# Performance work log

Measured on AMD Instinct MI355X. Metric: run time of the kernel, lower is better.

The kernel has to match this reference:

```python
import jax, jax.numpy as jnp
import numpy as np

DIM = 1024
CTX_DIM = 1024
HEADS = 16
DIM_HEAD = 64
INNER = HEADS * DIM_HEAD  # 1024
FF_INNER = 4 * DIM        # 4096
EPS = 1e-5


def layer_norm(x, g, b):
    mu = jnp.mean(x, axis=-1, keepdims=True)
    var = jnp.var(x, axis=-1, keepdims=True)
    return (x - mu) * jax.lax.rsqrt(var + EPS) * g + b


def setup_inputs() -> dict:
    key = jax.random.key(0)
    ks = jax.random.split(key, 9)
    b, n, j = 4, 2048, 1024
    inp = {
        "x": jax.random.normal(ks[0], (b, n, DIM), dtype=jnp.float32),
        "context": jax.random.normal(ks[1], (b, j, CTX_DIM), dtype=jnp.float32),
        "ln_g": jnp.ones((DIM,), jnp.float32),
        "ln_b": jnp.zeros((DIM,), jnp.float32),
        "cln_g": jnp.ones((CTX_DIM,), jnp.float32),
        "cln_b": jnp.zeros((CTX_DIM,), jnp.float32),
        "Wq": jax.random.normal(ks[2], (DIM, INNER), dtype=jnp.float32) * (DIM ** -0.5),
        "Wkv": jax.random.normal(ks[3], (CTX_DIM, 2 * DIM_HEAD), dtype=jnp.float32) * (CTX_DIM ** -0.5),
        "Wo": jax.random.normal(ks[4], (INNER, DIM), dtype=jnp.float32) * (INNER ** -0.5),
        "Wff1": jax.random.normal(ks[5], (DIM, 2 * FF_INNER), dtype=jnp.float32) * (DIM ** -0.5),
        "Wff2": jax.random.normal(ks[6], (FF_INNER, DIM), dtype=jnp.float32) * (FF_INNER ** -0.5),
    }
    return inp


def reference(x, context, ln_g, ln_b, cln_g, cln_b, Wq, Wkv, Wo, Wff1, Wff2):
    scale = DIM_HEAD ** -0.5
    xn = layer_norm(x, ln_g, ln_b)                       # [b, n, dim]
    cn = layer_norm(context, cln_g, cln_b)               # [b, j, ctx_dim]
    b, n, _ = xn.shape
    q = (xn @ Wq).reshape(b, n, HEADS, DIM_HEAD).transpose(0, 2, 1, 3) * scale  # [b,h,n,d]
    kv = cn @ Wkv                                        # [b, j, 2d]
    k, v = kv[..., :DIM_HEAD], kv[..., DIM_HEAD:]        # [b, j, d] each (shared head)
    sim = jnp.einsum('bhid,bjd->bhij', q, k)
    attn = jax.nn.softmax(sim, axis=-1)
    out = jnp.einsum('bhij,bjd->bhid', attn, v)          # [b,h,n,d]
    out = out.transpose(0, 2, 1, 3).reshape(b, n, INNER) @ Wo  # [b,n,dim]
    # parallel SwiGLU FF on normed x
    ff = xn @ Wff1                                       # [b,n,2*ff_inner]
    h, gate = ff[..., :FF_INNER], ff[..., FF_INNER:]
    out = out + (jax.nn.silu(gate) * h) @ Wff2
    return out
```

## Files before the change

### kernel.cpp

```cpp
#include <hip/hip_runtime.h>
#include <math.h>

typedef unsigned short u16;
typedef __attribute__((ext_vector_type(8))) short short8;
typedef __attribute__((ext_vector_type(8))) unsigned short ushortx8;
typedef __attribute__((ext_vector_type(4))) unsigned short ushortx4;
typedef __attribute__((ext_vector_type(4))) float floatx4;

#define DEVI __device__ __forceinline__

DEVI float bf2f(u16 u) {
    unsigned int i = ((unsigned int)u) << 16;
    float f; __builtin_memcpy(&f, &i, 4); return f;
}
DEVI u16 f2bf(float f) {
    unsigned int i; __builtin_memcpy(&i, &f, 4);
    i += 0x7fffu + ((i >> 16) & 1u);
    return (u16)(i >> 16);
}
DEVI void gl_lds16(const void* g, void* l) {
    __builtin_amdgcn_global_load_lds(
        (const __attribute__((address_space(1))) void*)g,
        (__attribute__((address_space(3))) void*)l, 16, 0, 0);
}

__global__ void transpose_kernel(const float* __restrict__ B, u16* __restrict__ BT,
                                 int K, int N) {
    __shared__ u16 t[32][33];
    int nb = blockIdx.x * 32, kb = blockIdx.y * 32;
    int tx = threadIdx.x, ty = threadIdx.y;
    for (int i = ty; i < 32; i += 8)
        t[i][tx] = f2bf(B[(size_t)(kb + i) * N + nb + tx]);
    __syncthreads();
    for (int i = ty; i < 32; i += 8)
        BT[(size_t)(nb + i) * K + kb + tx] = t[tx][i];
}

__global__ __launch_bounds__(256)
void ln_kernel(const float* __restrict__ x, const float* __restrict__ g,
               const float* __restrict__ b, u16* __restrict__ out) {
    __shared__ float sw[4], sw2[4];
    const int tid = threadIdx.x, wave = tid >> 6, lane = tid & 63;
    const float* xr = x + (size_t)blockIdx.x * 1024;
    float4 v = *(const float4*)(xr + tid * 4);
    float f[4] = {v.x, v.y, v.z, v.w};
    float s = f[0] + f[1] + f[2] + f[3];
    float s2 = f[0]*f[0] + f[1]*f[1] + f[2]*f[2] + f[3]*f[3];
    for (int o = 32; o; o >>= 1) {
        s  += __shfl_xor(s,  o, 64);
        s2 += __shfl_xor(s2, o, 64);
    }
    if (lane == 0) { sw[wave] = s; sw2[wave] = s2; }
    __syncthreads();
    float tot  = sw[0] + sw[1] + sw[2] + sw[3];
    float tot2 = sw2[0] + sw2[1] + sw2[2] + sw2[3];
    float mu  = tot * (1.f / 1024.f);
    float var = tot2 * (1.f / 1024.f) - mu * mu;
    float rs  = rsqrtf(var + 1e-5f);
    float4 gv = *(const float4*)(g + tid * 4);
    float4 bv = *(const float4*)(b + tid * 4);
    ushortx4 ov;
    ov[0] = f2bf((f[0] - mu) * rs * gv.x + bv.x);
    ov[1] = f2bf((f[1] - mu) * rs * gv.y + bv.y);
    ov[2] = f2bf((f[2] - mu) * rs * gv.z + bv.z);
    ov[3] = f2bf((f[3] - mu) * rs * gv.w + bv.w);
    *(ushortx4*)(out + (size_t)blockIdx.x * 1024 + tid * 4) = ov;
}

enum { EPI_PLAIN = 0, EPI_Q = 1, EPI_KV = 2, EPI_ADD_F32 = 3 };

template <int EPI>
__global__ __launch_bounds__(256)
void gemm_bt_kernel(const u16* __restrict__ A, const u16* __restrict__ BT,
                    void* __restrict__ Cv, u16* __restrict__ AUX,
                    int M, int N, int K) {
    __shared__ u16 As[128 * 32];
    __shared__ u16 Bs[128 * 32];
    const int tid = threadIdx.x, wave = tid >> 6, lane = tid & 63;
    const int mbase = blockIdx.x * 128, nbase = blockIdx.y * 128;
    const int m0 = (wave & 1) * 64, n0 = (wave >> 1) * 64;
    const int lrow = lane & 15, lq = lane >> 4;

    floatx4 zero = {0.f, 0.f, 0.f, 0.f};
    floatx4 acc[4][4];
#pragma unroll
    for (int i = 0; i < 4; i++)
#pragma unroll
        for (int j = 0; j < 4; j++) acc[i][j] = zero;

    for (int kt = 0; kt < K; kt += 32) {
#pragma unroll
        for (int i = 0; i < 2; i++) {
            int e = i * 2048 + tid * 8;
            int r = e >> 5, c = e & 31;
            gl_lds16(A  + (size_t)(mbase + r) * K + kt + c, As + e);
            gl_lds16(BT + (size_t)(nbase + r) * K + kt + c, Bs + e);
        }
        __syncthreads();
        short8 af[4], bf[4];
#pragma unroll
        for (int f = 0; f < 4; f++) {
            af[f] = *(const short8*)(As + (m0 + f * 16 + lrow) * 32 + lq * 8);
            bf[f] = *(const short8*)(Bs + (n0 + f * 16 + lrow) * 32 + lq * 8);
        }
#pragma unroll
        for (int i = 0; i < 4; i++)
#pragma unroll
            for (int j = 0; j < 4; j++)
                acc[i][j] = __builtin_amdgcn_mfma_f32_16x16x32_bf16(af[i], bf[j], acc[i][j], 0, 0, 0);
        __syncthreads();
    }

#pragma unroll
    for (int mf = 0; mf < 4; mf++)
#pragma unroll
        for (int nf = 0; nf < 4; nf++)
#pragma unroll
            for (int r = 0; r < 4; r++) {
                int row = mbase + m0 + mf * 16 + lq * 4 + r;
                int col = nbase + n0 + nf * 16 + lrow;
                float v = acc[mf][nf][r];
                if constexpr (EPI == EPI_PLAIN) {
                    ((u16*)Cv)[(size_t)row * N + col] = f2bf(v);
                } else if constexpr (EPI == EPI_Q) {
                    int b = row >> 11, i2 = row & 2047, h = col >> 6, d = col & 63;
                    ((u16*)Cv)[((size_t)((b * 16 + h) * 2048 + i2)) * 64 + d] = f2bf(v * 0.125f);
                } else if constexpr (EPI == EPI_KV) {
                    int b = row >> 10, j = row & 1023;
                    if (col < 64) ((u16*)Cv)[(size_t)row * 64 + col] = f2bf(v);
                    else AUX[((size_t)(b * 64 + (col - 64))) * 1024 + j] = f2bf(v);
                } else {
                    ((float*)Cv)[(size_t)row * N + col] = v + bf2f(AUX[(size_t)row * N + col]);
                }
            }
}

__global__ __launch_bounds__(256)
void gemm_ff1_kernel(const u16* __restrict__ A, const u16* __restrict__ BTh,
                     const u16* __restrict__ BTg, u16* __restrict__ Cact,
                     int K, int Nout) {
    __shared__ u16 As[128 * 32];
    __shared__ u16 Bh[64 * 32];
    __shared__ u16 Bg[64 * 32];
    const int tid = threadIdx.x, wave = tid >> 6, lane = tid & 63;
    const int mbase = blockIdx.x * 128, nbase = blockIdx.y * 64;
    const int m0 = (wave & 1) * 64, n0 = (wave >> 1) * 32;
    const int lrow = lane & 15, lq = lane >> 4;

    floatx4 zero = {0.f, 0.f, 0.f, 0.f};
    floatx4 ah[4][2], ag[4][2];
#pragma unroll
    for (int i = 0; i < 4; i++)
#pragma unroll
        for (int j = 0; j < 2; j++) { ah[i][j] = zero; ag[i][j] = zero; }

    for (int kt = 0; kt < K; kt += 32) {
#pragma unroll
        for (int i = 0; i < 2; i++) {
            int e = i * 2048 + tid * 8;
            int r = e >> 5, c = e & 31;
            gl_lds16(A + (size_t)(mbase + r) * K + kt + c, As + e);
        }
        {
            int e = tid * 8;
            int r = e >> 5, c = e & 31;
            gl_lds16(BTh + (size_t)(nbase + r) * K + kt + c, Bh + e);
            gl_lds16(BTg + (size_t)(nbase + r) * K + kt + c, Bg + e);
        }
        __syncthreads();
        short8 af[4], bhf[2], bgf[2];
#pragma unroll
        for (int f = 0; f < 4; f++)
            af[f] = *(const short8*)(As + (m0 + f * 16 + lrow) * 32 + lq * 8);
#pragma unroll
        for (int f = 0; f < 2; f++) {
            bhf[f] = *(const short8*)(Bh + (n0 + f * 16 + lrow) * 32 + lq * 8);
            bgf[f] = *(const short8*)(Bg + (n0 + f * 16 + lrow) * 32 + lq * 8);
        }
#pragma unroll
        for (int i = 0; i < 4; i++)
#pragma unroll
            for (int j = 0; j < 2; j++) {
                ah[i][j] = __builtin_amdgcn_mfma_f32_16x16x32_bf16(af[i], bhf[j], ah[i][j], 0, 0, 0);
                ag[i][j] = __builtin_amdgcn_mfma_f32_16x16x32_bf16(af[i], bgf[j], ag[i][j], 0, 0, 0);
            }
        __syncthreads();
    }

#pragma unroll
    for (int mf = 0; mf < 4; mf++)
#pragma unroll
        for (int nf = 0; nf < 2; nf++)
#pragma unroll
            for (int r = 0; r < 4; r++) {
                int row = mbase + m0 + mf * 16 + lq * 4 + r;
                int col = nbase + n0 + nf * 16 + lrow;
                float hv = ah[mf][nf][r], gv = ag[mf][nf][r];
                float act = hv * (gv / (1.f + __expf(-gv)));
                Cact[(size_t)row * Nout + col] = f2bf(act);
            }
}

__global__ __launch_bounds__(256)
void attn_kernel(const u16* __restrict__ q, const u16* __restrict__ k,
                 const u16* __restrict__ vt, u16* __restrict__ o) {
    __shared__ u16 Qs[64 * 72];
    __shared__ u16 Ks[128 * 72];
    __shared__ u16 VTs[64 * 136];
    __shared__ u16 Ps[64 * 136];
    __shared__ float Lp[4][64];
    __shared__ float Ltot[64];

    const int tid = threadIdx.x, wave = tid >> 6, lane = tid & 63;
    const int lrow = lane & 15, lq = lane >> 4;
    const int b = blockIdx.z, h = blockIdx.y, mt = blockIdx.x;

    const u16* qb = q + ((size_t)((b * 16 + h) * 2048) + mt * 64) * 64;
    const u16* kb = k + (size_t)b * 1024 * 64;
    const u16* vb = vt + (size_t)b * 64 * 1024;

#pragma unroll
    for (int i = 0; i < 2; i++) {
        int e = i * 2048 + tid * 8;
        int r = e >> 6, d = e & 63;
        *(ushortx8*)(Qs + r * 72 + d) = *(const ushortx8*)(qb + e);
    }

    floatx4 zero = {0.f, 0.f, 0.f, 0.f};
    floatx4 oacc[4];
#pragma unroll
    for (int i = 0; i < 4; i++) oacc[i] = zero;
    float lsum[4] = {0.f, 0.f, 0.f, 0.f};

    for (int jt = 0; jt < 8; jt++) {
#pragma unroll
        for (int i = 0; i < 4; i++) {
            int e = i * 2048 + tid * 8;
            int r = e >> 6, d = e & 63;
            *(ushortx8*)(Ks + r * 72 + d) = *(const ushortx8*)(kb + jt * 8192 + e);
            int dv = e >> 7, jj = e & 127;
            *(ushortx8*)(VTs + dv * 136 + jj) =
                *(const ushortx8*)(vb + (size_t)dv * 1024 + jt * 128 + jj);
        }
        __syncthreads();

        floatx4 sacc[2][4];
#pragma unroll
        for (int rf = 0; rf < 2; rf++)
#pragma unroll
            for (int cf = 0; cf < 4; cf++) sacc[rf][cf] = zero;
#pragma unroll
        for (int ks = 0; ks < 2; ks++) {
            short8 af[2], bfq[4];
#pragma unroll
            for (int rf = 0; rf < 2; rf++)
                af[rf] = *(const short8*)(Ks + (wave * 32 + rf * 16 + lrow) * 72 + ks * 32 + lq * 8);
#pragma unroll
            for (int cf = 0; cf < 4; cf++)
                bfq[cf] = *(const short8*)(Qs + (cf * 16 + lrow) * 72 + ks * 32 + lq * 8);
#pragma unroll
            for (int rf = 0; rf < 2; rf++)
#pragma unroll
                for (int cf = 0; cf < 4; cf++)
                    sacc[rf][cf] = __builtin_amdgcn_mfma_f32_16x16x32_bf16(af[rf], bfq[cf], sacc[rf][cf], 0, 0, 0);
        }

#pragma unroll
        for (int rf = 0; rf < 2; rf++)
#pragma unroll
            for (int cf = 0; cf < 4; cf++) {
                float p0 = __expf(sacc[rf][cf][0]);
                float p1 = __expf(sacc[rf][cf][1]);
                float p2 = __expf(sacc[rf][cf][2]);
                float p3 = __expf(sacc[rf][cf][3]);
                lsum[cf] += p0 + p1 + p2 + p3;
                ushortx4 pk = {f2bf(p0), f2bf(p1), f2bf(p2), f2bf(p3)};
                int m = cf * 16 + lrow;
                int j0 = wave * 32 + rf * 16 + lq * 4;
                *(ushortx4*)(Ps + m * 136 + j0) = pk;
            }
        __syncthreads();

#pragma unroll
        for (int ks = 0; ks < 4; ks++) {
            short8 pf[4];
#pragma unroll
            for (int mf = 0; mf < 4; mf++)
                pf[mf] = *(const short8*)(Ps + (mf * 16 + lrow) * 136 + ks * 32 + lq * 8);
            short8 vf = *(const short8*)(VTs + (wave * 16 + lrow) * 136 + ks * 32 + lq * 8);
#pragma unroll
            for (int mf = 0; mf < 4; mf++)
                oacc[mf] = __builtin_amdgcn_mfma_f32_16x16x32_bf16(pf[mf], vf, oacc[mf], 0, 0, 0);
        }
        __syncthreads();
    }

    float lv[4];
#pragma unroll
    for (int cf = 0; cf < 4; cf++) {
        float v = lsum[cf];
        v += __shfl_xor(v, 16, 64);
        v += __shfl_xor(v, 32, 64);
        lv[cf] = v;
    }
    if (lane < 16) {
#pragma unroll
        for (int cf = 0; cf < 4; cf++) Lp[wave][cf * 16 + lane] = lv[cf];
    }
    __syncthreads();
    if (tid < 64) Ltot[tid] = Lp[0][tid] + Lp[1][tid] + Lp[2][tid] + Lp[3][tid];
    __syncthreads();

    const int d = wave * 16 + lrow;
    const size_t orow0 = (size_t)(b * 2048 + mt * 64);
#pragma unroll
    for (int mf = 0; mf < 4; mf++)
#pragma unroll
        for (int r = 0; r < 4; r++) {
            int m = mf * 16 + lq * 4 + r;
            float val = oacc[mf][r] / Ltot[m];
            o[(orow0 + m) * 1024 + h * 64 + d] = f2bf(val);
        }
}

extern "C" void kernel_launch(void* const* d_in, const int* in_sizes, int n_in,
                              void* d_out, int out_size, void* d_ws, size_t ws_size,
                              hipStream_t stream) {
    const float* x     = (const float*)d_in[0];
    const float* ctx   = (const float*)d_in[1];
    const float* ln_g  = (const float*)d_in[2];
    const float* ln_b  = (const float*)d_in[3];
    const float* cln_g = (const float*)d_in[4];
    const float* cln_b = (const float*)d_in[5];
    const float* Wq    = (const float*)d_in[6];
    const float* Wkv   = (const float*)d_in[7];
    const float* Wo    = (const float*)d_in[8];
    const float* Wff1  = (const float*)d_in[9];
    const float* Wff2  = (const float*)d_in[10];
    (void)in_sizes; (void)n_in; (void)out_size; (void)ws_size;

    u16* ws = (u16*)d_ws;
    const size_t MiB = 524288;
    u16* ffa   = ws;
    u16* qb    = ws;
    u16* attnb = ws + 16 * MiB;
    u16* cn    = ws + 32 * MiB;
    u16* kb    = ws + 40 * MiB;
    u16* vtb   = ws + 40 * MiB + 262144;
    u16* WqT   = ws + 41 * MiB;
    u16* WkvT  = ws + 43 * MiB;
    u16* WoT   = ws + 44 * MiB;
    u16* xn    = ws + 64 * MiB;
    u16* wo    = ws + 80 * MiB;
    u16* Wff1T = ws + 96 * MiB;
    u16* Wff2T = ws + 112 * MiB;

    dim3 tb(32, 8);
    transpose_kernel<<<dim3(32, 32),  tb, 0, stream>>>(Wq,   WqT,   1024, 1024);
    transpose_kernel<<<dim3(4, 32),   tb, 0, stream>>>(Wkv,  WkvT,  1024, 128);
    transpose_kernel<<<dim3(32, 32),  tb, 0, stream>>>(Wo,   WoT,   1024, 1024);
    transpose_kernel<<<dim3(256, 32), tb, 0, stream>>>(Wff1, Wff1T, 1024, 8192);
    transpose_kernel<<<dim3(32, 128), tb, 0, stream>>>(Wff2, Wff2T, 4096, 1024);

    ln_kernel<<<8192, 256, 0, stream>>>(x,   ln_g,  ln_b,  xn);
    ln_kernel<<<4096, 256, 0, stream>>>(ctx, cln_g, cln_b, cn);

    gemm_bt_kernel<EPI_Q> <<<dim3(64, 8), 256, 0, stream>>>(xn, WqT,  qb, nullptr, 8192, 1024, 1024);
    gemm_bt_kernel<EPI_KV><<<dim3(32, 1), 256, 0, stream>>>(cn, WkvT, kb, vtb,     4096, 128,  1024);

    attn_kernel<<<dim3(32, 16, 4), 256, 0, stream>>>(qb, kb, vtb, attnb);

    gemm_bt_kernel<EPI_PLAIN><<<dim3(64, 8), 256, 0, stream>>>(attnb, WoT, wo, nullptr, 8192, 1024, 1024);
    gemm_ff1_kernel<<<dim3(64, 64), 256, 0, stream>>>(xn, Wff1T, Wff1T + (size_t)4096 * 1024, ffa, 1024, 4096);
    gemm_bt_kernel<EPI_ADD_F32><<<dim3(64, 8), 256, 0, stream>>>(ffa, Wff2T, d_out, wo, 8192, 1024, 4096);
}
```

Measured before the change: 622.4 us.

## Enlarge FF1 GEMM tile to 256 rows and cache Q fragments in attention

The FF1 GEMM now runs 512-thread blocks with a 256-row M tile, so each block shares the loaded B (h and gate) tiles across twice as many rows. B loading is split so half the threads fetch the h weights and half fetch the gate weights. In the attention kernel, Q fragments are loaded into registers once before the loop instead of being re-read from LDS every iteration, and LDS buffers are overlapped (Q with P, Lp with K) to shrink the footprint and raise occupancy. The cost is more register pressure from the held Q fragments, and fewer FF1 blocks in the grid.

```diff
diff --git a/kernel.cpp b/kernel.cpp
--- a/kernel.cpp
+++ b/kernel.cpp
@@ -135,16 +135,16 @@
             }
 }
 
-__global__ __launch_bounds__(256)
+__global__ __launch_bounds__(512)
 void gemm_ff1_kernel(const u16* __restrict__ A, const u16* __restrict__ BTh,
                      const u16* __restrict__ BTg, u16* __restrict__ Cact,
                      int K, int Nout) {
-    __shared__ u16 As[128 * 32];
+    __shared__ u16 As[256 * 32];
     __shared__ u16 Bh[64 * 32];
     __shared__ u16 Bg[64 * 32];
     const int tid = threadIdx.x, wave = tid >> 6, lane = tid & 63;
-    const int mbase = blockIdx.x * 128, nbase = blockIdx.y * 64;
-    const int m0 = (wave & 1) * 64, n0 = (wave >> 1) * 32;
+    const int mbase = blockIdx.x * 256, nbase = blockIdx.y * 64;
+    const int m0 = (wave & 3) * 64, n0 = (wave >> 2) * 32;
     const int lrow = lane & 15, lq = lane >> 4;
 
     floatx4 zero = {0.f, 0.f, 0.f, 0.f};
@@ -157,15 +157,16 @@
     for (int kt = 0; kt < K; kt += 32) {
 #pragma unroll
         for (int i = 0; i < 2; i++) {
-            int e = i * 2048 + tid * 8;
+            int e = i * 4096 + tid * 8;
             int r = e >> 5, c = e & 31;
             gl_lds16(A + (size_t)(mbase + r) * K + kt + c, As + e);
         }
         {
-            int e = tid * 8;
+            int e = (tid & 255) * 8;
             int r = e >> 5, c = e & 31;
-            gl_lds16(BTh + (size_t)(nbase + r) * K + kt + c, Bh + e);
-            gl_lds16(BTg + (size_t)(nbase + r) * K + kt + c, Bg + e);
+            const u16* src = (tid < 256) ? BTh : BTg;
+            u16* dst = (tid < 256) ? Bh : Bg;
+            gl_lds16(src + (size_t)(nbase + r) * K + kt + c, dst + e);
         }
         __syncthreads();
         short8 af[4], bhf[2], bgf[2];
@@ -204,12 +205,13 @@
 __global__ __launch_bounds__(256)
 void attn_kernel(const u16* __restrict__ q, const u16* __restrict__ k,
                  const u16* __restrict__ vt, u16* __restrict__ o) {
-    __shared__ u16 Qs[64 * 72];
-    __shared__ u16 Ks[128 * 72];
-    __shared__ u16 VTs[64 * 136];
-    __shared__ u16 Ps[64 * 136];
-    __shared__ float Lp[4][64];
-    __shared__ float Ltot[64];
+    __shared__ char smem[53248];
+    u16* Qs  = (u16*)smem;
+    u16* Ps  = (u16*)smem;
+    u16* Ks  = (u16*)(smem + 17408);
+    u16* VTs = (u16*)(smem + 35840);
+    float* Lp   = (float*)(smem + 17408);
+    float* Ltot = (float*)(smem + 18432);
 
     const int tid = threadIdx.x, wave = tid >> 6, lane = tid & 63;
     const int lrow = lane & 15, lq = lane >> 4;
@@ -225,6 +227,13 @@
         int r = e >> 6, d = e & 63;
         *(ushortx8*)(Qs + r * 72 + d) = *(const ushortx8*)(qb + e);
     }
+    __syncthreads();
+    short8 qf[2][4];
+#pragma unroll
+    for (int ks = 0; ks < 2; ks++)
+#pragma unroll
+        for (int cf = 0; cf < 4; cf++)
+            qf[ks][cf] = *(const short8*)(Qs + (cf * 16 + lrow) * 72 + ks * 32 + lq * 8);
 
     floatx4 zero = {0.f, 0.f, 0.f, 0.f};
     floatx4 oacc[4];
@@ -251,18 +260,15 @@
             for (int cf = 0; cf < 4; cf++) sacc[rf][cf] = zero;
 #pragma unroll
         for (int ks = 0; ks < 2; ks++) {
-            short8 af[2], bfq[4];
+            short8 af[2];
 #pragma unroll
             for (int rf = 0; rf < 2; rf++)
                 af[rf] = *(const short8*)(Ks + (wave * 32 + rf * 16 + lrow) * 72 + ks * 32 + lq * 8);
 #pragma unroll
-            for (int cf = 0; cf < 4; cf++)
-                bfq[cf] = *(const short8*)(Qs + (cf * 16 + lrow) * 72 + ks * 32 + lq * 8);
-#pragma unroll
             for (int rf = 0; rf < 2; rf++)
 #pragma unroll
                 for (int cf = 0; cf < 4; cf++)
-                    sacc[rf][cf] = __builtin_amdgcn_mfma_f32_16x16x32_bf16(af[rf], bfq[cf], sacc[rf][cf], 0, 0, 0);
+                    sacc[rf][cf] = __builtin_amdgcn_mfma_f32_16x16x32_bf16(af[rf], qf[ks][cf], sacc[rf][cf], 0, 0, 0);
         }
 
 #pragma unroll
@@ -305,10 +311,10 @@
     }
     if (lane < 16) {
 #pragma unroll
-        for (int cf = 0; cf < 4; cf++) Lp[wave][cf * 16 + lane] = lv[cf];
-    }
-    __syncthreads();
-    if (tid < 64) Ltot[tid] = Lp[0][tid] + Lp[1][tid] + Lp[2][tid] + Lp[3][tid];
+        for (int cf = 0; cf < 4; cf++) Lp[wave * 64 + cf * 16 + lane] = lv[cf];
+    }
+    __syncthreads();
+    if (tid < 64) Ltot[tid] = Lp[tid] + Lp[64 + tid] + Lp[128 + tid] + Lp[192 + tid];
     __syncthreads();
 
     const int d = wave * 16 + lrow;
@@ -371,6 +377,6 @@
     attn_kernel<<<dim3(32, 16, 4), 256, 0, stream>>>(qb, kb, vtb, attnb);
 
     gemm_bt_kernel<EPI_PLAIN><<<dim3(64, 8), 256, 0, stream>>>(attnb, WoT, wo, nullptr, 8192, 1024, 1024);
-    gemm_ff1_kernel<<<dim3(64, 64), 256, 0, stream>>>(xn, Wff1T, Wff1T + (size_t)4096 * 1024, ffa, 1024, 4096);
+    gemm_ff1_kernel<<<dim3(32, 64), 512, 0, stream>>>(xn, Wff1T, Wff1T + (size_t)4096 * 1024, ffa, 1024, 4096);
     gemm_bt_kernel<EPI_ADD_F32><<<dim3(64, 8), 256, 0, stream>>>(ffa, Wff2T, d_out, wo, 8192, 1024, 4096);
 }
```

Result: faster. 601.1 us (-3.4%).
